# Performance work log

Hardware: AMD Instinct MI355X
Metric: run time of the kernel (lower is better)

Reference implementation:

```python
import jax, jax.numpy as jnp
import numpy as np

D_MODEL = 1024
NUM_HEADS = 16
NUM_KV_HEADS = 4
D_K = D_MODEL // NUM_HEADS              # 64
G = NUM_HEADS // NUM_KV_HEADS           # queries per kv head = 4
B, S = 2, 2048


def setup_inputs() -> dict:
    key = jax.random.key(0)
    ks = jax.random.split(key, 11)
    s = 0.02
    return {
        "query": jax.random.normal(ks[0], (B, S, D_MODEL), jnp.float32),
        "key_in": jax.random.normal(ks[1], (B, S, D_MODEL), jnp.float32),
        "value_in": jax.random.normal(ks[2], (B, S, D_MODEL), jnp.float32),
        "Wq": jax.random.normal(ks[3], (D_MODEL, D_MODEL), jnp.float32) * s,
        "bq": jnp.zeros((D_MODEL,), jnp.float32),
        "Wk": jax.random.normal(ks[4], (D_MODEL, NUM_KV_HEADS * D_K), jnp.float32) * s,
        "bk": jnp.zeros((NUM_KV_HEADS * D_K,), jnp.float32),
        "Wv": jax.random.normal(ks[5], (D_MODEL, NUM_KV_HEADS * D_K), jnp.float32) * s,
        "bv": jnp.zeros((NUM_KV_HEADS * D_K,), jnp.float32),
        "Wo": jax.random.normal(ks[6], (D_MODEL, D_MODEL), jnp.float32) * s,
        "bo": jnp.zeros((D_MODEL,), jnp.float32),
    }


def reference(query, key_in, value_in, Wq, bq, Wk, bk, Wv, bv, Wo, bo):
    scale = jnp.sqrt(jnp.asarray(D_K, query.dtype))
    # Projections
    Q = (query @ Wq + bq).reshape(B, S, NUM_HEADS, D_K).transpose(0, 2, 1, 3)        # [B,H,S,dk]
    K = (key_in @ Wk + bk).reshape(B, S, NUM_KV_HEADS, D_K).transpose(0, 2, 1, 3)    # [B,KVH,S,dk]
    V = (value_in @ Wv + bv).reshape(B, S, NUM_KV_HEADS, D_K).transpose(0, 2, 1, 3)  # [B,KVH,S,dk]
    # repeat_interleave over head dim -> group Q heads by KV head instead
    Qg = Q.reshape(B, NUM_KV_HEADS, G, S, D_K)                                       # [B,KVH,G,S,dk]
    scores = jnp.einsum('bkgqd,bksd->bkgqs', Qg, K) / scale                          # [B,KVH,G,S,S]
    attn = jax.nn.softmax(scores, axis=-1)
    ctx = jnp.einsum('bkgqs,bksd->bkgqd', attn, V)                                   # [B,KVH,G,S,dk]
    ctx = ctx.reshape(B, NUM_HEADS, S, D_K).transpose(0, 2, 1, 3).reshape(B, S, D_MODEL)
    output = ctx @ Wo + bo
    # new_cache: K[:, ::G] on the repeated tensor == original K/V per kv head
    return output, K, V
```

## Files before the change

kernel.cpp:

```cpp
#include <hip/hip_runtime.h>

typedef unsigned short u16;
typedef unsigned int u32;
typedef __attribute__((ext_vector_type(8))) short short8;
typedef __attribute__((ext_vector_type(4))) float f32x4;

#define MFMA16(a, b, c) __builtin_amdgcn_mfma_f32_16x16x32_bf16(a, b, c, 0, 0, 0)

#define SEQ 2048
#define DM 1024

__device__ __forceinline__ u16 f2bf(float f) {
  u32 u = __float_as_uint(f);
  u += 0x7fffu + ((u >> 16) & 1u);
  return (u16)(u >> 16);
}
__device__ __forceinline__ u32 pack2(float a, float b) {
  return (u32)f2bf(a) | ((u32)f2bf(b) << 16);
}
__device__ __forceinline__ u32 pack2t(float a, float b) {
  return __builtin_amdgcn_perm(__float_as_uint(b), __float_as_uint(a), 0x07060302u);
}

template <bool F32>
__device__ __forceinline__ uint4 ld8(const void* p, size_t elem) {
  if constexpr (F32) {
    const float* f = (const float*)p + elem;
    float4 a = *(const float4*)f;
    float4 b = *(const float4*)(f + 4);
    uint4 r;
    r.x = pack2(a.x, a.y);
    r.y = pack2(a.z, a.w);
    r.z = pack2(b.x, b.y);
    r.w = pack2(b.z, b.w);
    return r;
  } else {
    return *(const uint4*)((const u16*)p + elem);
  }
}

__global__ void k_tr(const float* __restrict__ Wq, const float* __restrict__ Wk,
                     const float* __restrict__ Wv, const float* __restrict__ Wo,
                     u16* __restrict__ WqT, u16* __restrict__ WkT, u16* __restrict__ WvT,
                     u16* __restrict__ WoT) {
  const int z = blockIdx.z;
  const float* W = z == 0 ? Wq : (z == 1 ? Wk : (z == 2 ? Wv : Wo));
  u16* Wt = z == 0 ? WqT : (z == 1 ? WkT : (z == 2 ? WvT : WoT));
  const int N = (z == 1 || z == 2) ? 256 : 1024;
  const int n0 = blockIdx.x * 32;
  if (n0 >= N) return;
  const int k0 = blockIdx.y * 32;
  __shared__ float tile[32][33];
  int x = threadIdx.x & 31, y = threadIdx.x >> 5;
#pragma unroll
  for (int i = 0; i < 4; i++)
    tile[y + i * 8][x] = W[(size_t)(k0 + y + i * 8) * N + n0 + x];
  __syncthreads();
#pragma unroll
  for (int i = 0; i < 4; i++)
    Wt[(size_t)(n0 + y + i * 8) * 1024 + k0 + x] = f2bf(tile[x][y + i * 8]);
}

template <bool A32, bool B32>
__device__ __forceinline__ void gemm64(const void* __restrict__ A, const void* __restrict__ Bt,
                                       int m0, int n0, u16* lA, u16* lB, f32x4 acc[2][4]) {
  const int tid = threadIdx.x;
  const int lane = tid & 63, wave = tid >> 6;
  const int l15 = lane & 15, quad = lane >> 4;
  const int wm = wave >> 1, wn = wave & 1;
  const int sr = tid >> 3, scol = (tid & 7) * 8;
  f32x4 zero = {0.f, 0.f, 0.f, 0.f};
#pragma unroll
  for (int i = 0; i < 2; i++)
#pragma unroll
    for (int j = 0; j < 4; j++) acc[i][j] = zero;

  for (int k0 = 0; k0 < 1024; k0 += 64) {
#pragma unroll
    for (int it = 0; it < 2; it++) {
      int r = sr + it * 32;
      *(uint4*)&lA[r * 72 + scol] = ld8<A32>(A, (size_t)(m0 + r) * 1024 + k0 + scol);
    }
#pragma unroll
    for (int it = 0; it < 4; it++) {
      int r = sr + it * 32;
      *(uint4*)&lB[r * 72 + scol] = ld8<B32>(Bt, (size_t)(n0 + r) * 1024 + k0 + scol);
    }
    __syncthreads();
    short8 af[2][2], bfr[4][2];
#pragma unroll
    for (int i = 0; i < 2; i++)
#pragma unroll
      for (int kb = 0; kb < 2; kb++)
        af[i][kb] = *(const short8*)&lA[(wm * 32 + i * 16 + l15) * 72 + kb * 32 + quad * 8];
#pragma unroll
    for (int j = 0; j < 4; j++)
#pragma unroll
      for (int kb = 0; kb < 2; kb++)
        bfr[j][kb] = *(const short8*)&lB[(wn * 64 + j * 16 + l15) * 72 + kb * 32 + quad * 8];
#pragma unroll
    for (int i = 0; i < 2; i++)
#pragma unroll
      for (int j = 0; j < 4; j++) {
        acc[i][j] = MFMA16(af[i][0], bfr[j][0], acc[i][j]);
        acc[i][j] = MFMA16(af[i][1], bfr[j][1], acc[i][j]);
      }
    __syncthreads();
  }
}

__global__ __launch_bounds__(256) void k_proj(
    const float* __restrict__ query, const float* __restrict__ key_in,
    const float* __restrict__ value_in, const u16* __restrict__ WqT,
    const u16* __restrict__ WkT, const u16* __restrict__ WvT, const float* __restrict__ bq,
    const float* __restrict__ bk, const float* __restrict__ bv, u16* __restrict__ qbf,
    float* __restrict__ outK, u16* __restrict__ kbf, float* __restrict__ outV,
    u16* __restrict__ vtb, float qscale) {
  __shared__ u16 lA[64 * 72];
  __shared__ u16 lB[128 * 72];
  const int idx = blockIdx.x;
  const int lane = threadIdx.x & 63, wave = threadIdx.x >> 6;
  const int l15 = lane & 15, quad = lane >> 4;
  const int wm = wave >> 1, wn = wave & 1;
  f32x4 acc[2][4];

  if (idx < 640) {
    const u16* Wt;
    const float* act;
    const float* bias;
    int m0, n0, mode;
    if (idx < 512) {
      Wt = WqT; act = query; bias = bq; m0 = (idx >> 5) * 64; n0 = (idx & 31) * 128; mode = 0;
    } else {
      int i2 = idx - 512;
      Wt = WkT; act = key_in; bias = bk; m0 = (i2 >> 5) * 64; n0 = (i2 & 31) * 128; mode = 1;
    }
    gemm64<false, true>(Wt, act, m0, n0, lA, lB, acc);
#pragma unroll
    for (int i = 0; i < 2; i++) {
      int c0 = m0 + wm * 32 + i * 16 + quad * 4;
      float4 bb = *(const float4*)(bias + c0);
#pragma unroll
      for (int j = 0; j < 4; j++) {
        int token = n0 + wn * 64 + j * 16 + l15;
        int b = token >> 11, s = token & 2047;
        float v0 = acc[i][j][0] + bb.x, v1 = acc[i][j][1] + bb.y;
        float v2 = acc[i][j][2] + bb.z, v3 = acc[i][j][3] + bb.w;
        int d = c0 & 63;
        if (mode == 0) {
          int h = c0 >> 6;
          uint2 o;
          o.x = pack2(v0 * qscale, v1 * qscale);
          o.y = pack2(v2 * qscale, v3 * qscale);
          *(uint2*)(qbf + (((size_t)(b * 16 + h) * SEQ + s) << 6) + d) = o;
        } else {
          int kvh = c0 >> 6;
          size_t ix = (((size_t)(b * 4 + kvh) * SEQ + s) << 6) + d;
          float4 vv = {v0, v1, v2, v3};
          *(float4*)(outK + ix) = vv;
          uint2 o;
          o.x = pack2(v0, v1);
          o.y = pack2(v2, v3);
          *(uint2*)(kbf + ix) = o;
        }
      }
    }
  } else {
    int i2 = idx - 640;
    int m0 = (i2 >> 1) * 64, n0 = (i2 & 1) * 128;
    gemm64<true, false>(value_in, WvT, m0, n0, lA, lB, acc);
#pragma unroll
    for (int i = 0; i < 2; i++) {
      int r0 = m0 + wm * 32 + i * 16 + quad * 4;
      int b = r0 >> 11, s0 = r0 & 2047;
#pragma unroll
      for (int j = 0; j < 4; j++) {
        int col = n0 + wn * 64 + j * 16 + l15;
        int kvh = col >> 6, d = col & 63;
        float bv_ = bv[col];
        float v0 = acc[i][j][0] + bv_, v1 = acc[i][j][1] + bv_;
        float v2 = acc[i][j][2] + bv_, v3 = acc[i][j][3] + bv_;
        size_t base = (((size_t)(b * 4 + kvh) * SEQ + s0) << 6) + d;
        outV[base] = v0;
        outV[base + 64] = v1;
        outV[base + 128] = v2;
        outV[base + 192] = v3;
        uint2 o;
        o.x = pack2(v0, v1);
        o.y = pack2(v2, v3);
        *(uint2*)(vtb + ((size_t)(b * 4 + kvh) * 64 + d) * SEQ + s0) = o;
      }
    }
  }
}

__global__ __launch_bounds__(256) void k_out(const u16* __restrict__ ctxb,
                                             const u16* __restrict__ WoT,
                                             const float* __restrict__ bo,
                                             float* __restrict__ out) {
  __shared__ u16 lA[64 * 72];
  __shared__ u16 lB[128 * 72];
  const int idx = blockIdx.x;
  const int m0 = (idx >> 5) * 64, n0 = (idx & 31) * 128;
  const int lane = threadIdx.x & 63, wave = threadIdx.x >> 6;
  const int l15 = lane & 15, quad = lane >> 4;
  const int wm = wave >> 1, wn = wave & 1;
  f32x4 acc[2][4];
  gemm64<false, false>(WoT, ctxb, m0, n0, lA, lB, acc);
#pragma unroll
  for (int i = 0; i < 2; i++) {
    int c0 = m0 + wm * 32 + i * 16 + quad * 4;
    float4 bb = *(const float4*)(bo + c0);
#pragma unroll
    for (int j = 0; j < 4; j++) {
      int token = n0 + wn * 64 + j * 16 + l15;
      float4 vv = {acc[i][j][0] + bb.x, acc[i][j][1] + bb.y, acc[i][j][2] + bb.z,
                   acc[i][j][3] + bb.w};
      *(float4*)(out + (size_t)token * DM + c0) = vv;
    }
  }
}

__global__ __launch_bounds__(256, 4) void k_flash(const u16* __restrict__ Qh,
                                                  const u16* __restrict__ Kb,
                                                  const u16* __restrict__ Vt,
                                                  u16* __restrict__ ctx) {
  __shared__ u16 lK[128 * 64];
  __shared__ u16 lV[64 * 128];
  __shared__ u16 lP[4 * 16 * 64];
  const int tid = threadIdx.x;
  const int lane = tid & 63, wave = tid >> 6;
  const int l15 = lane & 15, quad = lane >> 4;
  const int bh = blockIdx.y;
  const int b = bh >> 4, h = bh & 15, kvh = h >> 2;
  const u16* Q = Qh + (size_t)bh * SEQ * 64;
  const u16* Kp = Kb + (size_t)(b * 4 + kvh) * SEQ * 64;
  const u16* Vp = Vt + (size_t)(b * 4 + kvh) * 64 * SEQ;
  const int q0 = blockIdx.x * 64 + wave * 16;

  short8 qf[2];
#pragma unroll
  for (int kb = 0; kb < 2; kb++)
    qf[kb] = *(const short8*)(Q + (size_t)(q0 + l15) * 64 + kb * 32 + quad * 8);

  short8 ones8;
  {
    short ov = (l15 == 0) ? (short)0x3F80 : (short)0;
    ones8 = (short8){ov, ov, ov, ov, ov, ov, ov, ov};
  }

  f32x4 zero = {0.f, 0.f, 0.f, 0.f};
  f32x4 acc[4];
  f32x4 lacc = zero;
#pragma unroll
  for (int n = 0; n < 4; n++) acc[n] = zero;

  u16* lPw = lP + wave * (16 * 64);
  const int t8 = tid * 8;

  for (int kc = 0; kc < SEQ; kc += 128) {
    __syncthreads();
#pragma unroll
    for (int i = 0; i < 4; i++) {
      int e = i * 2048 + t8;
      int row = e >> 6, ch = tid & 7;
      uint4 v = *(const uint4*)(Kp + (size_t)kc * 64 + e);
      *(uint4*)&lK[row * 64 + ((ch ^ (row & 7)) << 3)] = v;
    }
#pragma unroll
    for (int i = 0; i < 4; i++) {
      int e = i * 2048 + t8;
      int row = e >> 7, ch = tid & 15;
      uint4 v = *(const uint4*)(Vp + (size_t)row * SEQ + kc + ch * 8);
      *(uint4*)&lV[row * 128 + ((ch ^ (row & 15)) << 3)] = v;
    }
    __syncthreads();

#pragma unroll
    for (int sub = 0; sub < 2; sub++) {
      const int ks = sub * 64;
      f32x4 sc[4];
#pragma unroll
      for (int mt = 0; mt < 4; mt++) {
        int row = ks + mt * 16 + l15;
        short8 kf0 = *(const short8*)&lK[row * 64 + ((quad ^ (row & 7)) << 3)];
        short8 kf1 = *(const short8*)&lK[row * 64 + (((4 + quad) ^ (row & 7)) << 3)];
        f32x4 t = MFMA16(kf0, qf[0], zero);
        sc[mt] = MFMA16(kf1, qf[1], t);
      }
#pragma unroll
      for (int mt = 0; mt < 4; mt++) {
        float e0 = __builtin_amdgcn_exp2f(sc[mt][0]);
        float e1 = __builtin_amdgcn_exp2f(sc[mt][1]);
        float e2 = __builtin_amdgcn_exp2f(sc[mt][2]);
        float e3 = __builtin_amdgcn_exp2f(sc[mt][3]);
        int chp = mt * 2 + (quad >> 1);
        uint2 p;
        p.x = pack2t(e0, e1);
        p.y = pack2t(e2, e3);
        *(uint2*)&lPw[l15 * 64 + ((chp ^ (l15 & 7)) << 3) + (quad & 1) * 4] = p;
      }
      __asm__ volatile("s_waitcnt lgkmcnt(0)" ::: "memory");
#pragma unroll
      for (int kbp = 0; kbp < 2; kbp++) {
        int chq = kbp * 4 + quad;
        short8 pf = *(const short8*)&lPw[l15 * 64 + ((chq ^ (l15 & 7)) << 3)];
        lacc = MFMA16(ones8, pf, lacc);
#pragma unroll
        for (int n = 0; n < 4; n++) {
          int row = n * 16 + l15;
          int chv = sub * 8 + kbp * 4 + quad;
          short8 vf = *(const short8*)&lV[row * 128 + ((chv ^ (row & 15)) << 3)];
          acc[n] = MFMA16(vf, pf, acc[n]);
        }
      }
    }
  }

  float lq = __shfl(lacc[0], l15);
  float inv = __builtin_amdgcn_rcpf(lq);
  u16* base = ctx + ((size_t)(b * SEQ + q0 + l15)) * DM + h * 64;
#pragma unroll
  for (int n = 0; n < 4; n++) {
    uint2 o;
    o.x = pack2t(acc[n][0] * inv, acc[n][1] * inv);
    o.y = pack2t(acc[n][2] * inv, acc[n][3] * inv);
    *(uint2*)(base + n * 16 + quad * 4) = o;
  }
}

extern "C" void kernel_launch(void* const* d_in, const int* in_sizes, int n_in,
                              void* d_out, int out_size, void* d_ws, size_t ws_size,
                              hipStream_t stream) {
  const float* query = (const float*)d_in[0];
  const float* key_in = (const float*)d_in[1];
  const float* value_in = (const float*)d_in[2];
  const float* Wq = (const float*)d_in[3];
  const float* bq = (const float*)d_in[4];
  const float* Wk = (const float*)d_in[5];
  const float* bk = (const float*)d_in[6];
  const float* Wv = (const float*)d_in[7];
  const float* bv = (const float*)d_in[8];
  const float* Wo = (const float*)d_in[9];
  const float* bo = (const float*)d_in[10];

  float* out = (float*)d_out;
  float* outK = out + 4194304;
  float* outV = out + 5242880;

  char* ws = (char*)d_ws;
  u16* WqT = (u16*)(ws);
  u16* WkT = (u16*)(ws + 2097152);
  u16* WvT = (u16*)(ws + 2621440);
  u16* WoT = (u16*)(ws + 3145728);
  u16* qbf = (u16*)(ws + 5242880);
  u16* kbf = (u16*)(ws + 13631488);
  u16* vtb = (u16*)(ws + 15728640);
  u16* ctxb = (u16*)(ws + 17825792);

  const float qscale = 0.125f * 1.44269504088896340736f;

  k_tr<<<dim3(32, 32, 4), 256, 0, stream>>>(Wq, Wk, Wv, Wo, WqT, WkT, WvT, WoT);
  k_proj<<<dim3(768), 256, 0, stream>>>(query, key_in, value_in, WqT, WkT, WvT, bq, bk, bv,
                                        qbf, outK, kbf, outV, vtb, qscale);
  k_flash<<<dim3(32, 32), 256, 0, stream>>>(qbf, kbf, vtb, ctxb);
  k_out<<<dim3(512), 256, 0, stream>>>(ctxb, WoT, bo, out);
}
```

Before: 210.9 us.

## Use direct global-to-LDS loads with XOR-swizzled LDS layout in GEMM tiles

For bf16 operands, the GEMM tile loader now uses global_load_lds, which writes global data straight into shared memory without passing through registers. The LDS tiles drop their padding in favour of an XOR swizzle that avoids bank conflicts. fp32 operands are converted to bf16 with a hardware packed-convert instruction instead of manual rounding. Together these cut register traffic and the instruction count of the convert path. The trade-offs are reliance on the intrinsic's layout semantics and possible differences in rounding or NaN behaviour.

```diff
diff --git a/kernel.cpp b/kernel.cpp
--- a/kernel.cpp
+++ b/kernel.cpp
@@ -16,27 +16,26 @@
   return (u16)(u >> 16);
 }
 __device__ __forceinline__ u32 pack2(float a, float b) {
-  return (u32)f2bf(a) | ((u32)f2bf(b) << 16);
+  u32 r;
+  asm("v_cvt_pk_bf16_f32 %0, %1, %2" : "=v"(r) : "v"(a), "v"(b));
+  return r;
 }
 __device__ __forceinline__ u32 pack2t(float a, float b) {
   return __builtin_amdgcn_perm(__float_as_uint(b), __float_as_uint(a), 0x07060302u);
 }
-
-template <bool F32>
-__device__ __forceinline__ uint4 ld8(const void* p, size_t elem) {
-  if constexpr (F32) {
-    const float* f = (const float*)p + elem;
-    float4 a = *(const float4*)f;
-    float4 b = *(const float4*)(f + 4);
-    uint4 r;
-    r.x = pack2(a.x, a.y);
-    r.y = pack2(a.z, a.w);
-    r.z = pack2(b.x, b.y);
-    r.w = pack2(b.z, b.w);
-    return r;
-  } else {
-    return *(const uint4*)((const u16*)p + elem);
-  }
+__device__ __forceinline__ uint4 cvt8(const float* f) {
+  float4 a = *(const float4*)f;
+  float4 b = *(const float4*)(f + 4);
+  uint4 r;
+  r.x = pack2(a.x, a.y);
+  r.y = pack2(a.z, a.w);
+  r.z = pack2(b.x, b.y);
+  r.w = pack2(b.z, b.w);
+  return r;
+}
+__device__ __forceinline__ void gload16(const u16* g, u16* l) {
+  __builtin_amdgcn_global_load_lds((const __attribute__((address_space(1))) u32*)g,
+                                   (__attribute__((address_space(3))) u32*)l, 16, 0, 0);
 }
 
 __global__ void k_tr(const float* __restrict__ Wq, const float* __restrict__ Wk,
@@ -76,28 +75,58 @@
     for (int j = 0; j < 4; j++) acc[i][j] = zero;
 
   for (int k0 = 0; k0 < 1024; k0 += 64) {
-#pragma unroll
-    for (int it = 0; it < 2; it++) {
-      int r = sr + it * 32;
-      *(uint4*)&lA[r * 72 + scol] = ld8<A32>(A, (size_t)(m0 + r) * 1024 + k0 + scol);
-    }
-#pragma unroll
-    for (int it = 0; it < 4; it++) {
-      int r = sr + it * 32;
-      *(uint4*)&lB[r * 72 + scol] = ld8<B32>(Bt, (size_t)(n0 + r) * 1024 + k0 + scol);
+    if constexpr (A32) {
+      const float* Af = (const float*)A;
+#pragma unroll
+      for (int it = 0; it < 2; it++) {
+        int r = sr + it * 32;
+        uint4 v = cvt8(Af + (size_t)(m0 + r) * 1024 + k0 + scol);
+        *(uint4*)&lA[r * 64 + (((tid & 7) ^ (r & 7)) << 3)] = v;
+      }
+    } else {
+      const u16* Ab = (const u16*)A;
+#pragma unroll
+      for (int it = 0; it < 2; it++) {
+        int w8 = wave * 2 + it;
+        int r = w8 * 8 + (lane >> 3);
+        int g = (lane & 7) ^ (lane >> 3);
+        gload16(Ab + (size_t)(m0 + r) * 1024 + k0 + g * 8, &lA[w8 * 512]);
+      }
+    }
+    if constexpr (B32) {
+      const float* Bf = (const float*)Bt;
+#pragma unroll
+      for (int it = 0; it < 4; it++) {
+        int r = sr + it * 32;
+        uint4 v = cvt8(Bf + (size_t)(n0 + r) * 1024 + k0 + scol);
+        *(uint4*)&lB[r * 64 + (((tid & 7) ^ (r & 7)) << 3)] = v;
+      }
+    } else {
+      const u16* Bb = (const u16*)Bt;
+#pragma unroll
+      for (int it = 0; it < 4; it++) {
+        int w8 = wave * 4 + it;
+        int r = w8 * 8 + (lane >> 3);
+        int g = (lane & 7) ^ (lane >> 3);
+        gload16(Bb + (size_t)(n0 + r) * 1024 + k0 + g * 8, &lB[w8 * 512]);
+      }
     }
     __syncthreads();
     short8 af[2][2], bfr[4][2];
 #pragma unroll
     for (int i = 0; i < 2; i++)
 #pragma unroll
-      for (int kb = 0; kb < 2; kb++)
-        af[i][kb] = *(const short8*)&lA[(wm * 32 + i * 16 + l15) * 72 + kb * 32 + quad * 8];
+      for (int kb = 0; kb < 2; kb++) {
+        int r = wm * 32 + i * 16 + l15;
+        af[i][kb] = *(const short8*)&lA[r * 64 + (((kb * 4 + quad) ^ (r & 7)) << 3)];
+      }
 #pragma unroll
     for (int j = 0; j < 4; j++)
 #pragma unroll
-      for (int kb = 0; kb < 2; kb++)
-        bfr[j][kb] = *(const short8*)&lB[(wn * 64 + j * 16 + l15) * 72 + kb * 32 + quad * 8];
+      for (int kb = 0; kb < 2; kb++) {
+        int r = wn * 64 + j * 16 + l15;
+        bfr[j][kb] = *(const short8*)&lB[r * 64 + (((kb * 4 + quad) ^ (r & 7)) << 3)];
+      }
 #pragma unroll
     for (int i = 0; i < 2; i++)
 #pragma unroll
@@ -116,8 +145,8 @@
     const float* __restrict__ bk, const float* __restrict__ bv, u16* __restrict__ qbf,
     float* __restrict__ outK, u16* __restrict__ kbf, float* __restrict__ outV,
     u16* __restrict__ vtb, float qscale) {
-  __shared__ u16 lA[64 * 72];
-  __shared__ u16 lB[128 * 72];
+  __shared__ u16 lA[64 * 64];
+  __shared__ u16 lB[128 * 64];
   const int idx = blockIdx.x;
   const int lane = threadIdx.x & 63, wave = threadIdx.x >> 6;
   const int l15 = lane & 15, quad = lane >> 4;
@@ -198,8 +227,8 @@
                                              const u16* __restrict__ WoT,
                                              const float* __restrict__ bo,
                                              float* __restrict__ out) {
-  __shared__ u16 lA[64 * 72];
-  __shared__ u16 lB[128 * 72];
+  __shared__ u16 lA[64 * 64];
+  __shared__ u16 lB[128 * 64];
   const int idx = blockIdx.x;
   const int m0 = (idx >> 5) * 64, n0 = (idx & 31) * 128;
   const int lane = threadIdx.x & 63, wave = threadIdx.x >> 6;
```

Result: no change. 210.6 us (-0.2%).
